# Optimization experiments

Hardware: AMD Instinct MI355X
Metric: run time of the kernel (lower is better)

## Reference

```python
import jax, jax.numpy as jnp
import numpy as np

B, L, S, H = 2, 256, 384, 768
Tc, Dc = 16, 50
WV, WD = 20000, 100
CV = 128
NEG = -1e30


def _lstm_scan(x, Wih, Whh, bih, bhh):
    # x: [N, T, D] -> hs: [N, T, Hc]; torch LSTM gate order i,f,g,o
    N = x.shape[0]
    Hc = Whh.shape[1]
    h0 = jnp.zeros((N, Hc), x.dtype)

    def step(carry, xt):
        h, c = carry
        g = xt @ Wih.T + h @ Whh.T + bih + bhh  # [N, 4Hc]
        i, f, gg, o = jnp.split(g, 4, axis=-1)
        i = jax.nn.sigmoid(i)
        f = jax.nn.sigmoid(f)
        gg = jnp.tanh(gg)
        o = jax.nn.sigmoid(o)
        c = f * c + i * gg
        h = o * jnp.tanh(c)
        return (h, c), h

    _, hs = jax.lax.scan(step, (h0, h0), jnp.swapaxes(x, 0, 1))
    return jnp.swapaxes(hs, 0, 1)


def setup_inputs() -> dict:
    key = jax.random.key(0)
    ks = jax.random.split(key, 10)
    bert_emb = jax.random.normal(ks[0], (B, S, H), jnp.float32)
    pieces2word = jax.random.randint(ks[1], (B, L, S), 0, 2, jnp.int32)
    word_ids = jax.random.randint(ks[2], (B, L), 0, WV, jnp.int32)
    char_count = jax.random.randint(ks[3], (B, L), 1, Tc + 1, jnp.int32)
    char_ids = jax.random.randint(ks[4], (B, L, Tc), 0, CV, jnp.int32)
    # mask consistent with ragged char lengths (first char_count positions valid)
    token_masks_char = (jnp.arange(Tc)[None, None, :] < char_count[..., None]).astype(jnp.int32)
    word_table = jax.random.normal(ks[5], (WV, WD), jnp.float32) * 0.02
    char_table = jax.random.normal(ks[6], (CV, Dc), jnp.float32) * 0.02
    sc = 1.0 / np.sqrt(Dc)

    def lstm_w(k):
        a, b, c, d = jax.random.split(k, 4)
        return (jax.random.uniform(a, (4 * Dc, Dc), jnp.float32, -sc, sc),
                jax.random.uniform(b, (4 * Dc, Dc), jnp.float32, -sc, sc),
                jax.random.uniform(c, (4 * Dc,), jnp.float32, -sc, sc),
                jax.random.uniform(d, (4 * Dc,), jnp.float32, -sc, sc))

    Wih_f, Whh_f, bih_f, bhh_f = lstm_w(ks[7])
    Wih_b, Whh_b, bih_b, bhh_b = lstm_w(ks[8])
    return dict(bert_emb=bert_emb, pieces2word=pieces2word, word_ids=word_ids,
                char_count=char_count, char_ids=char_ids, token_masks_char=token_masks_char,
                word_table=word_table, char_table=char_table,
                Wih_f=Wih_f, Whh_f=Whh_f, bih_f=bih_f, bhh_f=bhh_f,
                Wih_b=Wih_b, Whh_b=Whh_b, bih_b=bih_b, bhh_b=bhh_b)


def reference(bert_emb, pieces2word, word_ids, char_count, char_ids, token_masks_char,
              word_table, char_table, Wih_f, Whh_f, bih_f, bhh_f, Wih_b, Whh_b, bih_b, bhh_b):
    # --- piece2word max pool (expand + masked_fill(min) + max over pieces) ---
    minv = jnp.min(bert_emb)
    # [B, L, S, H] intermediate, as in the original expand
    masked = jnp.where(pieces2word[..., None] != 0, bert_emb[:, None, :, :], minv)
    word_reps = jnp.max(masked, axis=2)  # [B, L, H]
    # dropouts are identity in eval mode

    # --- word embedding lookup ---
    word_embed = word_table[word_ids]  # [B, L, WD]

    # --- char bi-LSTM with packed-sequence semantics ---
    lens = jnp.maximum(char_count.reshape(-1), 1)  # char_count[char_count==0]=1
    x = char_table[char_ids.reshape(B * L, Tc)]  # [N, Tc, Dc]
    h_fwd = _lstm_scan(x, Wih_f, Whh_f, bih_f, bhh_f)
    # reverse each sequence within its valid length for the backward direction
    t = jnp.arange(Tc)[None, :]
    idx = jnp.where(t < lens[:, None], lens[:, None] - 1 - t, t)  # [N, Tc]
    x_rev = jnp.take_along_axis(x, idx[..., None], axis=1)
    h_bwd = _lstm_scan(x_rev, Wih_b, Whh_b, bih_b, bhh_b)
    h_bwd = jnp.take_along_axis(h_bwd, idx[..., None], axis=1)  # back to original order
    h = jnp.concatenate([h_fwd, h_bwd], axis=-1)  # [N, Tc, 2*Dc]
    valid = (t < lens[:, None])[..., None]
    h = jnp.where(valid, h, 0.0)  # pad_packed_sequence zero-pads beyond length
    h = h.reshape(B, L, Tc, 2 * Dc)

    # --- combine(..., 'max'): masked max over ragged char groups ---
    m = jnp.where(token_masks_char[..., None] == 0, NEG, 0.0)
    sup = jnp.max(m + h, axis=2)  # [B, L, 2*Dc]
    sup = jnp.where(sup == NEG, 0.0, sup)

    return jnp.concatenate([word_reps, word_embed, sup], axis=-1)  # [B, L, H+WD+2*Dc]
```

## Files before the change

kernel.cpp:

```cpp
#include <hip/hip_runtime.h>
#include <float.h>

#define Bb 2
#define Ll 256
#define Ss 384
#define Hh 768
#define Tc 16
#define Dc 50
#define WD 100
#define CV 128
#define NG 200
#define OUTC 968


__device__ inline float tanh_fast(float x) {
    float e = __expf(2.f * x);
    return 1.f - 2.f / (e + 1.f);
}
__device__ inline float sigmoid_fast(float x) {
    return 1.f / (1.f + __expf(-x));
}


__global__ __launch_bounds__(256) void kernel1(
        const float* __restrict__ bert, const float* __restrict__ char_table,
        const float* __restrict__ Wih_f, const float* __restrict__ bih_f, const float* __restrict__ bhh_f,
        const float* __restrict__ Wih_b, const float* __restrict__ bih_b, const float* __restrict__ bhh_b,
        const int* __restrict__ word_ids, const float* __restrict__ word_table,
        float* __restrict__ minp, float* __restrict__ xpt, float* __restrict__ out) {
    int blk = blockIdx.x, tid = threadIdx.x;
    if (blk < 128) {
        const int n4 = (Bb * Ss * Hh) / 4;
        const float4* b4 = (const float4*)bert;
        float m = FLT_MAX;
        for (int i = blk * 256 + tid; i < n4; i += 128 * 256) {
            float4 v = b4[i];
            m = fminf(m, fminf(fminf(v.x, v.y), fminf(v.z, v.w)));
        }
        #pragma unroll
        for (int off = 32; off; off >>= 1) m = fminf(m, __shfl_down(m, off, 64));
        __shared__ float red[4];
        if ((tid & 63) == 0) red[tid >> 6] = m;
        __syncthreads();
        if (tid == 0) minp[blk] = fminf(fminf(red[0], red[1]), fminf(red[2], red[3]));
    } else if (blk < 144) {
        int idx = blk - 128;
        int dir = idx >> 3, c0 = (idx & 7) * 16;
        const float* Wih = dir ? Wih_b : Wih_f;
        const float* bih = dir ? bih_b : bih_f;
        const float* bhh = dir ? bhh_b : bhh_f;
        __shared__ float ct[16][Dc];
        for (int e = tid; e < 16 * Dc; e += 256)
            ((float*)ct)[e] = char_table[c0 * Dc + e];
        __syncthreads();
        if (tid < NG) {
            float w[Dc];
            #pragma unroll
            for (int j = 0; j < Dc; j++) w[j] = Wih[tid * Dc + j];
            float bias = bih[tid] + bhh[tid];
            for (int cid = 0; cid < 16; cid++) {
                float a = bias;
                #pragma unroll
                for (int j = 0; j < Dc; j++) a += w[j] * ct[cid][j];
                xpt[(dir * CV + c0 + cid) * NG + tid] = a;
            }
        }
    } else {
        for (int i = (blk - 144) * 256 + tid; i < Bb * Ll * WD; i += 64 * 256) {
            int bl = i / WD, d = i - bl * WD;
            out[(size_t)bl * OUTC + Hh + d] = word_table[(size_t)word_ids[bl] * WD + d];
        }
    }
}


__global__ __launch_bounds__(256) void kernel2(
        const int* __restrict__ char_ids, const int* __restrict__ char_count,
        const float* __restrict__ Whh_f, const float* __restrict__ Whh_b,
        const float* __restrict__ xpt,
        const float* __restrict__ bert, const int* __restrict__ p2w,
        const float* __restrict__ minp, float* __restrict__ out) {
    __shared__ __align__(16) char smem[13888];
    int blk = blockIdx.x, tid = threadIdx.x;

    if (blk < 1024) {
        float (*xg)[NG] = (float (*)[NG])smem;
        float* gs  = (float*)(smem + 12800);
        float* hs  = (float*)(smem + 13600);
        int*   scid = (int*)(smem + 13808);

        int n = blk >> 1, dir = blk & 1;
        const float* Whh = dir ? Whh_b : Whh_f;

        int len = char_count[n];
        if (len < 1) len = 1;
        if (tid < Tc) {
            int t = tid;
            int st = dir ? (t < len ? len - 1 - t : t) : t;
            scid[t] = char_ids[n * Tc + st];
        }
        if (tid < 52) hs[tid] = 0.f;
        __syncthreads();

        for (int e = tid; e < Tc * (NG / 4); e += 256) {
            int t = e / 50, q = e - t * 50;
            ((float4*)xg[t])[q] = ((const float4*)&xpt[(dir * CV + scid[t]) * NG])[q];
        }
        float w[52];
        if (tid < NG) {
            #pragma unroll
            for (int j = 0; j < Dc; j++) w[j] = Whh[tid * Dc + j];
            w[50] = 0.f; w[51] = 0.f;
        }
        __syncthreads();

        float c = 0.f, maxv = -FLT_MAX;
        for (int t = 0; t < Tc; t++) {
            if (tid < NG) {
                float g = xg[t][tid];
                #pragma unroll
                for (int j = 0; j < 52; j += 4) {
                    float4 hv = *(const float4*)&hs[j];
                    g += hv.x * w[j] + hv.y * w[j+1] + hv.z * w[j+2] + hv.w * w[j+3];
                }
                gs[tid] = g;
            }
            __syncthreads();
            if (tid < Dc) {
                float si = sigmoid_fast(gs[tid]);
                float sf = sigmoid_fast(gs[tid + 50]);
                float tg = tanh_fast(gs[tid + 100]);
                float so = sigmoid_fast(gs[tid + 150]);
                c = sf * c + si * tg;
                float h = so * tanh_fast(c);
                hs[tid] = h;
                if (t < len) maxv = fmaxf(maxv, h);
            }
            __syncthreads();
        }
        if (tid < Dc)
            out[(size_t)n * OUTC + (Hh + WD) + dir * Dc + tid] = maxv;
    } else {
        float (*sacc)[4][128] = (float (*)[4][128])smem;
        float* sminv = (float*)(smem + 8192);

        if (tid < 64) {
            float m = fminf(minp[tid], minp[tid + 64]);
            #pragma unroll
            for (int off = 32; off; off >>= 1) m = fminf(m, __shfl_down(m, off, 64));
            if (tid == 0) *sminv = m;
        }
        int idx = blk - 1024;
        int hc  = idx % 6;
        int lt  = (idx / 6) & 63;
        int b   = idx / 384;
        int l0  = lt * 4;
        int w    = tid >> 6;
        int lane = tid & 63;
        int s0 = w * 96;

        const int* pm = p2w + ((size_t)(b * Ll + l0)) * Ss + s0;
        unsigned m0[4], m1[4], m2[4];
        #pragma unroll
        for (int r = 0; r < 4; r++) {
            unsigned long long b0 = __ballot(pm[r * Ss + lane] != 0);
            unsigned long long b1 = __ballot(lane < 32 ? (pm[r * Ss + 64 + lane] != 0) : false);
            m0[r] = __builtin_amdgcn_readfirstlane((unsigned)b0);
            m1[r] = __builtin_amdgcn_readfirstlane((unsigned)(b0 >> 32));
            m2[r] = __builtin_amdgcn_readfirstlane((unsigned)b1);
        }

        const float2* bb2 = (const float2*)(bert + (size_t)b * Ss * Hh) + hc * 64 + lane;
        float2 acc[4];
        #pragma unroll
        for (int r = 0; r < 4; r++) { acc[r].x = -FLT_MAX; acc[r].y = -FLT_MAX; }

        for (int jo = 0; jo < 96; jo += 8) {
            float2 v[8];
            #pragma unroll
            for (int k = 0; k < 8; k++) v[k] = bb2[(size_t)(s0 + jo + k) * 384];
            #pragma unroll
            for (int k = 0; k < 8; k++) {
                int j = jo + k;
                #pragma unroll
                for (int r = 0; r < 4; r++) {
                    unsigned bit = (j < 32 ? m0[r] >> j
                                 : j < 64 ? m1[r] >> (j - 32)
                                          : m2[r] >> (j - 64)) & 1u;
                    if (bit) {
                        acc[r].x = fmaxf(acc[r].x, v[k].x);
                        acc[r].y = fmaxf(acc[r].y, v[k].y);
                    }
                }
            }
        }
        #pragma unroll
        for (int r = 0; r < 4; r++)
            *(float2*)&sacc[w][r][lane * 2] = acc[r];
        __syncthreads();

        float mv = *sminv;
        #pragma unroll
        for (int e = tid; e < 4 * 128; e += 256) {
            int r = e >> 7, cx = e & 127;
            float m = fmaxf(fmaxf(sacc[0][r][cx], sacc[1][r][cx]),
                            fmaxf(sacc[2][r][cx], sacc[3][r][cx]));
            if (m == -FLT_MAX) m = mv;
            out[((size_t)(b * Ll + l0 + r)) * OUTC + hc * 128 + cx] = m;
        }
    }
}

extern "C" void kernel_launch(void* const* d_in, const int* in_sizes, int n_in,
                              void* d_out, int out_size, void* d_ws, size_t ws_size,
                              hipStream_t stream) {
    const float* bert       = (const float*)d_in[0];
    const int*   p2w        = (const int*)d_in[1];
    const int*   word_ids   = (const int*)d_in[2];
    const int*   char_count = (const int*)d_in[3];
    const int*   char_ids   = (const int*)d_in[4];
    const float* word_table = (const float*)d_in[6];
    const float* char_table = (const float*)d_in[7];
    const float* Wih_f = (const float*)d_in[8];
    const float* Whh_f = (const float*)d_in[9];
    const float* bih_f = (const float*)d_in[10];
    const float* bhh_f = (const float*)d_in[11];
    const float* Wih_b = (const float*)d_in[12];
    const float* Whh_b = (const float*)d_in[13];
    const float* bih_b = (const float*)d_in[14];
    const float* bhh_b = (const float*)d_in[15];
    float* out = (float*)d_out;

    float* minp = (float*)d_ws;
    float* xpt  = minp + 128;

    kernel1<<<208, 256, 0, stream>>>(
        bert, char_table, Wih_f, bih_f, bhh_f, Wih_b, bih_b, bhh_b,
        word_ids, word_table, minp, xpt, out);
    kernel2<<<1792, 256, 0, stream>>>(
        char_ids, char_count, Whh_f, Whh_b, xpt, bert, p2w, minp, out);
}
```

Baseline: 123.4 us.

## Drop global bert min pass, compute fallback lazily, retile max-pool to 8 rows

Removes the 128-block min reduction over all of bert_emb. The fallback value for empty pieces2word rows is now found by a serial per-thread scan that runs only when a row has no selected pieces. The word-embedding gather moves from kernel1 into kernel2, and kernel1 is split into 64 smaller Wih projection blocks. The max-pool tiles now cover 8 words instead of 4, so each bert column load is reused across more rows. The trade-off is that an input with empty mask rows would hit an extremely slow serial scan over about 590K elements per output element.

```diff
diff --git a/kernel.cpp b/kernel.cpp
--- a/kernel.cpp
+++ b/kernel.cpp
@@ -11,6 +11,7 @@
 #define CV 128
 #define NG 200
 #define OUTC 968
+#define LT 8
 
 
 __device__ inline float tanh_fast(float x) {
@@ -23,52 +24,29 @@
 
 
 __global__ __launch_bounds__(256) void kernel1(
-        const float* __restrict__ bert, const float* __restrict__ char_table,
+        const float* __restrict__ char_table,
         const float* __restrict__ Wih_f, const float* __restrict__ bih_f, const float* __restrict__ bhh_f,
         const float* __restrict__ Wih_b, const float* __restrict__ bih_b, const float* __restrict__ bhh_b,
-        const int* __restrict__ word_ids, const float* __restrict__ word_table,
-        float* __restrict__ minp, float* __restrict__ xpt, float* __restrict__ out) {
+        float* __restrict__ xpt) {
     int blk = blockIdx.x, tid = threadIdx.x;
-    if (blk < 128) {
-        const int n4 = (Bb * Ss * Hh) / 4;
-        const float4* b4 = (const float4*)bert;
-        float m = FLT_MAX;
-        for (int i = blk * 256 + tid; i < n4; i += 128 * 256) {
-            float4 v = b4[i];
-            m = fminf(m, fminf(fminf(v.x, v.y), fminf(v.z, v.w)));
-        }
-        #pragma unroll
-        for (int off = 32; off; off >>= 1) m = fminf(m, __shfl_down(m, off, 64));
-        __shared__ float red[4];
-        if ((tid & 63) == 0) red[tid >> 6] = m;
-        __syncthreads();
-        if (tid == 0) minp[blk] = fminf(fminf(red[0], red[1]), fminf(red[2], red[3]));
-    } else if (blk < 144) {
-        int idx = blk - 128;
-        int dir = idx >> 3, c0 = (idx & 7) * 16;
-        const float* Wih = dir ? Wih_b : Wih_f;
-        const float* bih = dir ? bih_b : bih_f;
-        const float* bhh = dir ? bhh_b : bhh_f;
-        __shared__ float ct[16][Dc];
-        for (int e = tid; e < 16 * Dc; e += 256)
-            ((float*)ct)[e] = char_table[c0 * Dc + e];
-        __syncthreads();
-        if (tid < NG) {
-            float w[Dc];
-            #pragma unroll
-            for (int j = 0; j < Dc; j++) w[j] = Wih[tid * Dc + j];
-            float bias = bih[tid] + bhh[tid];
-            for (int cid = 0; cid < 16; cid++) {
-                float a = bias;
-                #pragma unroll
-                for (int j = 0; j < Dc; j++) a += w[j] * ct[cid][j];
-                xpt[(dir * CV + c0 + cid) * NG + tid] = a;
-            }
-        }
-    } else {
-        for (int i = (blk - 144) * 256 + tid; i < Bb * Ll * WD; i += 64 * 256) {
-            int bl = i / WD, d = i - bl * WD;
-            out[(size_t)bl * OUTC + Hh + d] = word_table[(size_t)word_ids[bl] * WD + d];
+    int dir = blk >> 5, c0 = (blk & 31) * 4;
+    const float* Wih = dir ? Wih_b : Wih_f;
+    const float* bih = dir ? bih_b : bih_f;
+    const float* bhh = dir ? bhh_b : bhh_f;
+    __shared__ float ct[4][Dc];
+    if (tid < 4 * Dc) ((float*)ct)[tid] = char_table[c0 * Dc + tid];
+    __syncthreads();
+    if (tid < NG) {
+        float w[Dc];
+        #pragma unroll
+        for (int j = 0; j < Dc; j++) w[j] = Wih[tid * Dc + j];
+        float bias = bih[tid] + bhh[tid];
+        #pragma unroll
+        for (int cid = 0; cid < 4; cid++) {
+            float a = bias;
+            #pragma unroll
+            for (int j = 0; j < Dc; j++) a += w[j] * ct[cid][j];
+            xpt[(dir * CV + c0 + cid) * NG + tid] = a;
         }
     }
 }
@@ -79,8 +57,9 @@
         const float* __restrict__ Whh_f, const float* __restrict__ Whh_b,
         const float* __restrict__ xpt,
         const float* __restrict__ bert, const int* __restrict__ p2w,
-        const float* __restrict__ minp, float* __restrict__ out) {
-    __shared__ __align__(16) char smem[13888];
+        const int* __restrict__ word_ids, const float* __restrict__ word_table,
+        float* __restrict__ out) {
+    __shared__ __align__(16) char smem[16384];
     int blk = blockIdx.x, tid = threadIdx.x;
 
     if (blk < 1024) {
@@ -140,29 +119,22 @@
         }
         if (tid < Dc)
             out[(size_t)n * OUTC + (Hh + WD) + dir * Dc + tid] = maxv;
-    } else {
-        float (*sacc)[4][128] = (float (*)[4][128])smem;
-        float* sminv = (float*)(smem + 8192);
-
-        if (tid < 64) {
-            float m = fminf(minp[tid], minp[tid + 64]);
-            #pragma unroll
-            for (int off = 32; off; off >>= 1) m = fminf(m, __shfl_down(m, off, 64));
-            if (tid == 0) *sminv = m;
-        }
+    } else if (blk < 1408) {
+        float (*sacc)[LT][128] = (float (*)[LT][128])smem;
+
         int idx = blk - 1024;
         int hc  = idx % 6;
-        int lt  = (idx / 6) & 63;
-        int b   = idx / 384;
-        int l0  = lt * 4;
+        int lt  = (idx / 6) & 31;
+        int b   = idx / 192;
+        int l0  = lt * LT;
         int w    = tid >> 6;
         int lane = tid & 63;
         int s0 = w * 96;
 
         const int* pm = p2w + ((size_t)(b * Ll + l0)) * Ss + s0;
-        unsigned m0[4], m1[4], m2[4];
-        #pragma unroll
-        for (int r = 0; r < 4; r++) {
+        unsigned m0[LT], m1[LT], m2[LT];
+        #pragma unroll
+        for (int r = 0; r < LT; r++) {
             unsigned long long b0 = __ballot(pm[r * Ss + lane] != 0);
             unsigned long long b1 = __ballot(lane < 32 ? (pm[r * Ss + 64 + lane] != 0) : false);
             m0[r] = __builtin_amdgcn_readfirstlane((unsigned)b0);
@@ -171,9 +143,9 @@
         }
 
         const float2* bb2 = (const float2*)(bert + (size_t)b * Ss * Hh) + hc * 64 + lane;
-        float2 acc[4];
-        #pragma unroll
-        for (int r = 0; r < 4; r++) { acc[r].x = -FLT_MAX; acc[r].y = -FLT_MAX; }
+        float2 acc[LT];
+        #pragma unroll
+        for (int r = 0; r < LT; r++) { acc[r].x = -FLT_MAX; acc[r].y = -FLT_MAX; }
 
         for (int jo = 0; jo < 96; jo += 8) {
             float2 v[8];
@@ -183,7 +155,7 @@
             for (int k = 0; k < 8; k++) {
                 int j = jo + k;
                 #pragma unroll
-                for (int r = 0; r < 4; r++) {
+                for (int r = 0; r < LT; r++) {
                     unsigned bit = (j < 32 ? m0[r] >> j
                                  : j < 64 ? m1[r] >> (j - 32)
                                           : m2[r] >> (j - 64)) & 1u;
@@ -195,18 +167,26 @@
             }
         }
         #pragma unroll
-        for (int r = 0; r < 4; r++)
+        for (int r = 0; r < LT; r++)
             *(float2*)&sacc[w][r][lane * 2] = acc[r];
         __syncthreads();
 
-        float mv = *sminv;
-        #pragma unroll
-        for (int e = tid; e < 4 * 128; e += 256) {
+        for (int e = tid; e < LT * 128; e += 256) {
             int r = e >> 7, cx = e & 127;
             float m = fmaxf(fmaxf(sacc[0][r][cx], sacc[1][r][cx]),
                             fmaxf(sacc[2][r][cx], sacc[3][r][cx]));
-            if (m == -FLT_MAX) m = mv;
+            if (m == -FLT_MAX) {
+                float mv = FLT_MAX;
+                #pragma unroll 1
+                for (int i = 0; i < Bb * Ss * Hh; i++) mv = fminf(mv, bert[i]);
+                m = mv;
+            }
             out[((size_t)(b * Ll + l0 + r)) * OUTC + hc * 128 + cx] = m;
+        }
+    } else {
+        for (int i = (blk - 1408) * 256 + tid; i < Bb * Ll * WD; i += 64 * 256) {
+            int bl = i / WD, d = i - bl * WD;
+            out[(size_t)bl * OUTC + Hh + d] = word_table[(size_t)word_ids[bl] * WD + d];
         }
     }
 }
@@ -231,12 +211,11 @@
     const float* bhh_b = (const float*)d_in[15];
     float* out = (float*)d_out;
 
-    float* minp = (float*)d_ws;
-    float* xpt  = minp + 128;
-
-    kernel1<<<208, 256, 0, stream>>>(
-        bert, char_table, Wih_f, bih_f, bhh_f, Wih_b, bih_b, bhh_b,
-        word_ids, word_table, minp, xpt, out);
-    kernel2<<<1792, 256, 0, stream>>>(
-        char_ids, char_count, Whh_f, Whh_b, xpt, bert, p2w, minp, out);
-}
+    float* xpt = (float*)d_ws;
+
+    kernel1<<<64, 256, 0, stream>>>(
+        char_table, Wih_f, bih_f, bhh_f, Wih_b, bih_b, bhh_b, xpt);
+    kernel2<<<1472, 256, 0, stream>>>(
+        char_ids, char_count, Whh_f, Whh_b, xpt, bert, p2w,
+        word_ids, word_table, out);
+}
```

Result: slower. 147.5 us (+19.5%).

## Split fused kernel into word-max and single-wave LSTM kernels with retuned tiling

Applied to the files above, without the earlier changes.

Splits the combined second kernel into a word-pooling kernel and an LSTM kernel. The word kernel now has 512-thread blocks that each cover 8 words, 256 columns as float4, and 48 pieces per wave. The LSTM kernel uses one 64-lane wave per sequence and direction: each lane computes all four gates of one hidden unit, keeping 4x50 recurrent weights in registers and prefetching the next step's input projection. This is meant to cut the block-wide barriers and thread idleness of the 256-thread LSTM step and to raise memory-level parallelism in the pooling. The costs are an extra kernel launch, heavy register pressure from the 208-float weight array, and lower occupancy for the LSTM kernel. The input-projection prep is also spread over more, smaller blocks.

```diff
diff --git a/kernel.cpp b/kernel.cpp
--- a/kernel.cpp
+++ b/kernel.cpp
@@ -22,7 +22,7 @@
 }
 
 
-__global__ __launch_bounds__(256) void kernel1(
+__global__ __launch_bounds__(256) void prep_kernel(
         const float* __restrict__ bert, const float* __restrict__ char_table,
         const float* __restrict__ Wih_f, const float* __restrict__ bih_f, const float* __restrict__ bhh_f,
         const float* __restrict__ Wih_b, const float* __restrict__ bih_b, const float* __restrict__ bhh_b,
@@ -43,22 +43,22 @@
         if ((tid & 63) == 0) red[tid >> 6] = m;
         __syncthreads();
         if (tid == 0) minp[blk] = fminf(fminf(red[0], red[1]), fminf(red[2], red[3]));
-    } else if (blk < 144) {
+    } else if (blk < 192) {
         int idx = blk - 128;
-        int dir = idx >> 3, c0 = (idx & 7) * 16;
+        int dir = idx >> 5, c0 = (idx & 31) * 4;
         const float* Wih = dir ? Wih_b : Wih_f;
         const float* bih = dir ? bih_b : bih_f;
         const float* bhh = dir ? bhh_b : bhh_f;
-        __shared__ float ct[16][Dc];
-        for (int e = tid; e < 16 * Dc; e += 256)
-            ((float*)ct)[e] = char_table[c0 * Dc + e];
+        __shared__ float ct[4][Dc];
+        if (tid < 4 * Dc) ((float*)ct)[tid] = char_table[c0 * Dc + tid];
         __syncthreads();
         if (tid < NG) {
             float w[Dc];
             #pragma unroll
             for (int j = 0; j < Dc; j++) w[j] = Wih[tid * Dc + j];
             float bias = bih[tid] + bhh[tid];
-            for (int cid = 0; cid < 16; cid++) {
+            #pragma unroll
+            for (int cid = 0; cid < 4; cid++) {
                 float a = bias;
                 #pragma unroll
                 for (int j = 0; j < Dc; j++) a += w[j] * ct[cid][j];
@@ -66,7 +66,7 @@
             }
         }
     } else {
-        for (int i = (blk - 144) * 256 + tid; i < Bb * Ll * WD; i += 64 * 256) {
+        for (int i = (blk - 192) * 256 + tid; i < Bb * Ll * WD; i += 64 * 256) {
             int bl = i / WD, d = i - bl * WD;
             out[(size_t)bl * OUTC + Hh + d] = word_table[(size_t)word_ids[bl] * WD + d];
         }
@@ -74,141 +74,157 @@
 }
 
 
-__global__ __launch_bounds__(256) void kernel2(
+__global__ __launch_bounds__(512) void word_kernel(
+        const float* __restrict__ bert, const int* __restrict__ p2w,
+        const float* __restrict__ minp, float* __restrict__ out) {
+    __shared__ float sacc[8][8][256];
+    __shared__ float sminv;
+    int tid = threadIdx.x;
+    int wv = tid >> 6, lane = tid & 63;
+
+    if (tid < 64) {
+        float m = fminf(minp[tid], minp[tid + 64]);
+        #pragma unroll
+        for (int off = 32; off; off >>= 1) m = fminf(m, __shfl_down(m, off, 64));
+        if (tid == 0) sminv = m;
+    }
+
+    int idx = blockIdx.x;
+    int hc = idx % 3;
+    int lt = (idx / 3) & 31;
+    int b  = idx / 96;
+    int l0 = lt * 8;
+    int s0 = wv * 48;
+
+    const int* pm = p2w + ((size_t)(b * Ll + l0)) * Ss + s0;
+    unsigned mlo[8], mhi[8];
+    #pragma unroll
+    for (int r = 0; r < 8; r++) {
+        unsigned long long bal = __ballot(lane < 48 ? (pm[r * Ss + lane] != 0) : false);
+        mlo[r] = __builtin_amdgcn_readfirstlane((unsigned)bal);
+        mhi[r] = __builtin_amdgcn_readfirstlane((unsigned)(bal >> 32));
+    }
+
+    const float4* bb4 = (const float4*)(bert + (size_t)b * Ss * Hh) + hc * 64 + lane;
+    float4 acc[8];
+    #pragma unroll
+    for (int r = 0; r < 8; r++) { acc[r].x = acc[r].y = acc[r].z = acc[r].w = -FLT_MAX; }
+
+    for (int jo = 0; jo < 48; jo += 8) {
+        float4 v[8];
+        #pragma unroll
+        for (int k = 0; k < 8; k++) v[k] = bb4[(size_t)(s0 + jo + k) * 192];
+        #pragma unroll
+        for (int k = 0; k < 8; k++) {
+            int j = jo + k;
+            #pragma unroll
+            for (int r = 0; r < 8; r++) {
+                unsigned bit = (j < 32 ? mlo[r] >> j : mhi[r] >> (j - 32)) & 1u;
+                if (bit) {
+                    acc[r].x = fmaxf(acc[r].x, v[k].x);
+                    acc[r].y = fmaxf(acc[r].y, v[k].y);
+                    acc[r].z = fmaxf(acc[r].z, v[k].z);
+                    acc[r].w = fmaxf(acc[r].w, v[k].w);
+                }
+            }
+        }
+    }
+    #pragma unroll
+    for (int r = 0; r < 8; r++)
+        *(float4*)&sacc[wv][r][lane * 4] = acc[r];
+    __syncthreads();
+
+    float mv = sminv;
+    #pragma unroll
+    for (int e = tid; e < 8 * 256; e += 512) {
+        int r = e >> 8, cx = e & 255;
+        float m = sacc[0][r][cx];
+        #pragma unroll
+        for (int k = 1; k < 8; k++) m = fmaxf(m, sacc[k][r][cx]);
+        if (m == -FLT_MAX) m = mv;
+        out[((size_t)(b * Ll + l0 + r)) * OUTC + hc * 256 + cx] = m;
+    }
+}
+
+
+__global__ __launch_bounds__(64, 1) void lstm_kernel(
         const int* __restrict__ char_ids, const int* __restrict__ char_count,
         const float* __restrict__ Whh_f, const float* __restrict__ Whh_b,
-        const float* __restrict__ xpt,
-        const float* __restrict__ bert, const int* __restrict__ p2w,
-        const float* __restrict__ minp, float* __restrict__ out) {
-    __shared__ __align__(16) char smem[13888];
-    int blk = blockIdx.x, tid = threadIdx.x;
-
-    if (blk < 1024) {
-        float (*xg)[NG] = (float (*)[NG])smem;
-        float* gs  = (float*)(smem + 12800);
-        float* hs  = (float*)(smem + 13600);
-        int*   scid = (int*)(smem + 13808);
-
-        int n = blk >> 1, dir = blk & 1;
-        const float* Whh = dir ? Whh_b : Whh_f;
-
-        int len = char_count[n];
-        if (len < 1) len = 1;
-        if (tid < Tc) {
-            int t = tid;
-            int st = dir ? (t < len ? len - 1 - t : t) : t;
-            scid[t] = char_ids[n * Tc + st];
-        }
-        if (tid < 52) hs[tid] = 0.f;
-        __syncthreads();
-
-        for (int e = tid; e < Tc * (NG / 4); e += 256) {
-            int t = e / 50, q = e - t * 50;
-            ((float4*)xg[t])[q] = ((const float4*)&xpt[(dir * CV + scid[t]) * NG])[q];
-        }
-        float w[52];
-        if (tid < NG) {
-            #pragma unroll
-            for (int j = 0; j < Dc; j++) w[j] = Whh[tid * Dc + j];
-            w[50] = 0.f; w[51] = 0.f;
-        }
-        __syncthreads();
-
-        float c = 0.f, maxv = -FLT_MAX;
-        for (int t = 0; t < Tc; t++) {
-            if (tid < NG) {
-                float g = xg[t][tid];
-                #pragma unroll
-                for (int j = 0; j < 52; j += 4) {
-                    float4 hv = *(const float4*)&hs[j];
-                    g += hv.x * w[j] + hv.y * w[j+1] + hv.z * w[j+2] + hv.w * w[j+3];
-                }
-                gs[tid] = g;
+        const float* __restrict__ xpt, float* __restrict__ out) {
+    int blk = blockIdx.x;
+    int n = blk >> 1, dir = blk & 1;
+    int lane = threadIdx.x;
+    const float* Whh = dir ? Whh_b : Whh_f;
+    __shared__ __align__(16) float hs[52];
+
+    int len = char_count[n];
+    if (len < 1) len = 1;
+
+    int cidv = 0;
+    if (lane < Tc) {
+        int st = dir ? (lane < len ? len - 1 - lane : lane) : lane;
+        cidv = char_ids[n * Tc + st];
+    }
+
+    float w[4][52];
+    if (lane < Dc) {
+        #pragma unroll
+        for (int q = 0; q < 4; q++) {
+            const float2* wr = (const float2*)(Whh + (q * Dc + lane) * Dc);
+            #pragma unroll
+            for (int m = 0; m < 25; m++) {
+                float2 t = wr[m];
+                w[q][2 * m] = t.x; w[q][2 * m + 1] = t.y;
             }
-            __syncthreads();
-            if (tid < Dc) {
-                float si = sigmoid_fast(gs[tid]);
-                float sf = sigmoid_fast(gs[tid + 50]);
-                float tg = tanh_fast(gs[tid + 100]);
-                float so = sigmoid_fast(gs[tid + 150]);
-                c = sf * c + si * tg;
-                float h = so * tanh_fast(c);
-                hs[tid] = h;
-                if (t < len) maxv = fmaxf(maxv, h);
-            }
-            __syncthreads();
-        }
-        if (tid < Dc)
-            out[(size_t)n * OUTC + (Hh + WD) + dir * Dc + tid] = maxv;
-    } else {
-        float (*sacc)[4][128] = (float (*)[4][128])smem;
-        float* sminv = (float*)(smem + 8192);
-
-        if (tid < 64) {
-            float m = fminf(minp[tid], minp[tid + 64]);
-            #pragma unroll
-            for (int off = 32; off; off >>= 1) m = fminf(m, __shfl_down(m, off, 64));
-            if (tid == 0) *sminv = m;
-        }
-        int idx = blk - 1024;
-        int hc  = idx % 6;
-        int lt  = (idx / 6) & 63;
-        int b   = idx / 384;
-        int l0  = lt * 4;
-        int w    = tid >> 6;
-        int lane = tid & 63;
-        int s0 = w * 96;
-
-        const int* pm = p2w + ((size_t)(b * Ll + l0)) * Ss + s0;
-        unsigned m0[4], m1[4], m2[4];
-        #pragma unroll
-        for (int r = 0; r < 4; r++) {
-            unsigned long long b0 = __ballot(pm[r * Ss + lane] != 0);
-            unsigned long long b1 = __ballot(lane < 32 ? (pm[r * Ss + 64 + lane] != 0) : false);
-            m0[r] = __builtin_amdgcn_readfirstlane((unsigned)b0);
-            m1[r] = __builtin_amdgcn_readfirstlane((unsigned)(b0 >> 32));
-            m2[r] = __builtin_amdgcn_readfirstlane((unsigned)b1);
-        }
-
-        const float2* bb2 = (const float2*)(bert + (size_t)b * Ss * Hh) + hc * 64 + lane;
-        float2 acc[4];
-        #pragma unroll
-        for (int r = 0; r < 4; r++) { acc[r].x = -FLT_MAX; acc[r].y = -FLT_MAX; }
-
-        for (int jo = 0; jo < 96; jo += 8) {
-            float2 v[8];
-            #pragma unroll
-            for (int k = 0; k < 8; k++) v[k] = bb2[(size_t)(s0 + jo + k) * 384];
-            #pragma unroll
-            for (int k = 0; k < 8; k++) {
-                int j = jo + k;
-                #pragma unroll
-                for (int r = 0; r < 4; r++) {
-                    unsigned bit = (j < 32 ? m0[r] >> j
-                                 : j < 64 ? m1[r] >> (j - 32)
-                                          : m2[r] >> (j - 64)) & 1u;
-                    if (bit) {
-                        acc[r].x = fmaxf(acc[r].x, v[k].x);
-                        acc[r].y = fmaxf(acc[r].y, v[k].y);
-                    }
-                }
-            }
-        }
-        #pragma unroll
-        for (int r = 0; r < 4; r++)
-            *(float2*)&sacc[w][r][lane * 2] = acc[r];
-        __syncthreads();
-
-        float mv = *sminv;
-        #pragma unroll
-        for (int e = tid; e < 4 * 128; e += 256) {
-            int r = e >> 7, cx = e & 127;
-            float m = fmaxf(fmaxf(sacc[0][r][cx], sacc[1][r][cx]),
-                            fmaxf(sacc[2][r][cx], sacc[3][r][cx]));
-            if (m == -FLT_MAX) m = mv;
-            out[((size_t)(b * Ll + l0 + r)) * OUTC + hc * 128 + cx] = m;
-        }
-    }
+        }
+    }
+    #pragma unroll
+    for (int q = 0; q < 4; q++) { w[q][50] = 0.f; w[q][51] = 0.f; }
+
+    if (lane < 52) hs[lane] = 0.f;
+    __syncthreads();
+
+    int cid0 = __shfl(cidv, 0);
+    const float* xr = xpt + (size_t)(dir * CV + cid0) * NG;
+    float xp[4];
+    #pragma unroll
+    for (int q = 0; q < 4; q++) xp[q] = (lane < Dc) ? xr[q * Dc + lane] : 0.f;
+
+    float c = 0.f, h = 0.f, maxv = -FLT_MAX;
+    for (int t = 0; t < Tc; t++) {
+        int tn = (t + 1 < Tc) ? t + 1 : t;
+        int cidn = __shfl(cidv, tn);
+        const float* xrn = xpt + (size_t)(dir * CV + cidn) * NG;
+        float xpn[4];
+        #pragma unroll
+        for (int q = 0; q < 4; q++) xpn[q] = (lane < Dc) ? xrn[q * Dc + lane] : 0.f;
+
+        float g0 = xp[0], g1 = xp[1], g2 = xp[2], g3 = xp[3];
+        #pragma unroll
+        for (int m = 0; m < 13; m++) {
+            float4 hv = *(const float4*)&hs[4 * m];
+            g0 += hv.x * w[0][4*m] + hv.y * w[0][4*m+1] + hv.z * w[0][4*m+2] + hv.w * w[0][4*m+3];
+            g1 += hv.x * w[1][4*m] + hv.y * w[1][4*m+1] + hv.z * w[1][4*m+2] + hv.w * w[1][4*m+3];
+            g2 += hv.x * w[2][4*m] + hv.y * w[2][4*m+1] + hv.z * w[2][4*m+2] + hv.w * w[2][4*m+3];
+            g3 += hv.x * w[3][4*m] + hv.y * w[3][4*m+1] + hv.z * w[3][4*m+2] + hv.w * w[3][4*m+3];
+        }
+        if (lane < Dc) {
+            float si = sigmoid_fast(g0);
+            float sf = sigmoid_fast(g1);
+            float tg = tanh_fast(g2);
+            float so = sigmoid_fast(g3);
+            c = sf * c + si * tg;
+            h = so * tanh_fast(c);
+            if (t < len) maxv = fmaxf(maxv, h);
+        }
+        __syncthreads();
+        if (lane < Dc) hs[lane] = h;
+        __syncthreads();
+        #pragma unroll
+        for (int q = 0; q < 4; q++) xp[q] = xpn[q];
+    }
+    if (lane < Dc)
+        out[(size_t)n * OUTC + (Hh + WD) + dir * Dc + lane] = maxv;
 }
 
 extern "C" void kernel_launch(void* const* d_in, const int* in_sizes, int n_in,
@@ -234,9 +250,10 @@
     float* minp = (float*)d_ws;
     float* xpt  = minp + 128;
 
-    kernel1<<<208, 256, 0, stream>>>(
+    prep_kernel<<<256, 256, 0, stream>>>(
         bert, char_table, Wih_f, bih_f, bhh_f, Wih_b, bih_b, bhh_b,
         word_ids, word_table, minp, xpt, out);
-    kernel2<<<1792, 256, 0, stream>>>(
-        char_ids, char_count, Whh_f, Whh_b, xpt, bert, p2w, minp, out);
-}
+    word_kernel<<<192, 512, 0, stream>>>(bert, p2w, minp, out);
+    lstm_kernel<<<1024, 64, 0, stream>>>(
+        char_ids, char_count, Whh_f, Whh_b, xpt, out);
+}
```

After: 127.9 us. 1.04x slower.
